# Optimization experiments

Measured on AMD Instinct MI355X. Metric: run time of the kernel, lower is better.

Reference implementation:

```python
import jax, jax.numpy as jnp
import numpy as np

# Config mirrors Model(d_model=512, output_dim=2); RetNet(num_layers=2, n_heads=1)
D_MODEL = 512
N_LAYERS = 2
OUT_DIM = 2
B, S = 16, 1024
GAMMA = 1.0 - 2.0 ** -5  # RetNet decay for head 0 (n_heads=1)
EPS = 1e-6


def setup_inputs() -> dict:
    key = jax.random.key(0)
    ks = jax.random.split(key, 10)
    d, L = D_MODEL, N_LAYERS

    def rn(k, shape, scale):
        return jax.random.normal(k, shape, dtype=jnp.float32) * scale

    return {
        "x": rn(ks[0], (B, S, d), 1.0),
        # per-layer retention projections, stacked on a leading layer axis
        "Wq": rn(ks[1], (L, d, d), d ** -0.5),
        "Wk": rn(ks[2], (L, d, d), d ** -0.5),
        "Wv": rn(ks[3], (L, d, d), d ** -0.5),
        "Wg": rn(ks[4], (L, d, d), d ** -0.5),
        "Wo": rn(ks[5], (L, d, d), d ** -0.5),
        # pre-norm LayerNorm affine params
        "ln1_g": jnp.ones((L, d), jnp.float32),
        "ln1_b": jnp.zeros((L, d), jnp.float32),
        "ln2_g": jnp.ones((L, d), jnp.float32),
        "ln2_b": jnp.zeros((L, d), jnp.float32),
        # FFN (hidden = 2*d_model, gelu) per RetNet paper
        "W1": rn(ks[6], (L, d, 2 * d), d ** -0.5),
        "b1": jnp.zeros((L, 2 * d), jnp.float32),
        "W2": rn(ks[7], (L, 2 * d, d), (2 * d) ** -0.5),
        "b2": jnp.zeros((L, d), jnp.float32),
        # readout Linear(d_model, output_dim)
        "Wro": rn(ks[8], (d, OUT_DIM), d ** -0.5),
        "bro": jnp.zeros((OUT_DIM,), jnp.float32),
    }


def _layer_norm(x, g, b):
    mu = jnp.mean(x, axis=-1, keepdims=True)
    var = jnp.var(x, axis=-1, keepdims=True)
    return (x - mu) * jax.lax.rsqrt(var + EPS) * g + b


def _retention(x, Wq, Wk, Wv, Wg, Wo):
    # single head: d_head = d_model
    d = x.shape[-1]
    q = x @ Wq                      # [B,S,d]
    k = (x @ Wk) * (d ** -0.5)      # scaled keys
    v = x @ Wv
    n = jnp.arange(x.shape[1])
    diff = n[:, None] - n[None, :]
    # D[n,m] = gamma^(n-m) for n >= m else 0 (causal decay mask)
    D = jnp.where(diff >= 0, jnp.exp(diff.astype(jnp.float32) * np.log(GAMMA)), 0.0)
    scores = jnp.einsum("bnd,bmd->bnm", q, k) * D       # [B,S,S]
    ret = jnp.einsum("bnm,bmd->bnd", scores, v)          # [B,S,d]
    # GroupNorm over the (single) head dim, no affine
    mu = jnp.mean(ret, axis=-1, keepdims=True)
    var = jnp.var(ret, axis=-1, keepdims=True)
    ret = (ret - mu) * jax.lax.rsqrt(var + EPS)
    # swish gate + output projection
    return (jax.nn.silu(x @ Wg) * ret) @ Wo


def reference(x, Wq, Wk, Wv, Wg, Wo, ln1_g, ln1_b, ln2_g, ln2_b, W1, b1, W2, b2, Wro, bro):
    h = x
    for l in range(N_LAYERS):  # small fixed layer count
        h = h + _retention(_layer_norm(h, ln1_g[l], ln1_b[l]), Wq[l], Wk[l], Wv[l], Wg[l], Wo[l])
        y = _layer_norm(h, ln2_g[l], ln2_b[l])
        h = h + jax.nn.gelu(y @ W1[l] + b1[l]) @ W2[l] + b2[l]
    pooled = h.sum(axis=1)          # [B,d] sum pooling over sequence
    return pooled @ Wro + bro       # [B,OUT_DIM]
```

## Files before the change

kernel.cpp:

```cpp
#include <hip/hip_runtime.h>
#include <hip/hip_bf16.h>


#define D_MODEL 512
#define SEQ 1024
#define BATCH 16
#define NROWS (BATCH * SEQ)
#define HID 1024
#define LOG2_GAMMA (-0.04580368961f)
#define KSCALE (0.044194173824f)

typedef __attribute__((ext_vector_type(8))) short bf16x8;
typedef __attribute__((ext_vector_type(4))) float f32x4;

__device__ inline unsigned short f2bf(float x) {
    union { float f; unsigned u; } uu; uu.f = x;
    unsigned r = uu.u + 0x7fff + ((uu.u >> 16) & 1);
    return (unsigned short)(r >> 16);
}
__device__ inline float bf2f(unsigned short x) {
    union { unsigned u; float f; } uu; uu.u = ((unsigned)x) << 16; return uu.f;
}

__device__ inline void gload_lds16(const void* g, void* l) {
    __builtin_amdgcn_global_load_lds(
        (const __attribute__((address_space(1))) void*)g,
        (__attribute__((address_space(3))) void*)l, 16, 0, 0);
}

__device__ inline float sigm(float z) {
    return 1.f / (1.f + exp2f(z * -1.442695040888963f));
}
__device__ inline float gelu_fast(float x) {
    float y = 1.5957691216057308f * (x + 0.044715f * x * x * x);
    return x * sigm(y);
}

template <int EPI>
__global__ __launch_bounds__(512, 2) void gemm256p(
    const short* __restrict__ A, const short* __restrict__ B,
    const float* __restrict__ bias, unsigned short* __restrict__ C,
    int K, int lda, int ldb, int ldc, int nbx) {
    __shared__ __align__(16) short smem[4 * 16384];
    const int tid = threadIdx.x;
    const int lane = tid & 63;
    const int wid = tid >> 6;
    const int wm = wid >> 2, wn = wid & 3;
    const int cpx = gridDim.x >> 3;
    const int wg = ((int)blockIdx.x & 7) * cpx + ((int)blockIdx.x >> 3);
    const int m0 = (wg / nbx) * 256;
    const int n0 = (wg % nbx) * 256;

    const int srow = tid >> 2;
    const int scol = (((tid & 3) ^ ((tid >> 3) & 3)) * 8);
    auto stage = [&](int slot, int t) {
        int k0 = t * 32;
#pragma unroll
        for (int r = 0; r < 2; ++r) {
            gload_lds16(A + (long long)(m0 + r * 128 + srow) * lda + k0 + scol,
                        &smem[slot * 16384 + r * 4096 + wid * 512]);
            gload_lds16(B + (long long)(n0 + r * 128 + srow) * ldb + k0 + scol,
                        &smem[slot * 16384 + 8192 + r * 4096 + wid * 512]);
        }
    };

    const int NT = K >> 5;
    f32x4 acc[8][4] = {};
    const int sw8 = (((lane >> 4) ^ ((lane >> 1) & 3)) * 8);
    const int aoff = (wm * 128 + (lane & 15)) * 32 + sw8;
    const int boff = 8192 + (wn * 64 + (lane & 15)) * 32 + sw8;

    bf16x8 aR0[8], bR0[4], aR1[8], bR1[4];
    stage(0, 0); stage(1, 1); stage(2, 2);
    asm volatile("s_waitcnt vmcnt(8)" ::: "memory");
    __builtin_amdgcn_s_barrier();
#pragma unroll
    for (int m = 0; m < 8; ++m) aR0[m] = *(const bf16x8*)&smem[aoff + m * 512];
#pragma unroll
    for (int n = 0; n < 4; ++n) bR0[n] = *(const bf16x8*)&smem[boff + n * 512];

#define STEP256(T, AC, BC, AN, BN2)                                                   \
    {                                                                                 \
        int t = (T);                                                                  \
        if (t + 3 < NT) stage((t + 3) & 3, t + 3);                                    \
        if (t + 3 < NT)      asm volatile("s_waitcnt vmcnt(8)" ::: "memory");         \
        else if (t + 2 < NT) asm volatile("s_waitcnt vmcnt(4)" ::: "memory");         \
        else if (t + 1 < NT) asm volatile("s_waitcnt vmcnt(0)" ::: "memory");         \
        __builtin_amdgcn_s_barrier();                                                 \
        const int sb = ((t + 1) & 3) * 16384;                                         \
        const bool pre = (t + 1 < NT);                                                \
        _Pragma("unroll")                                                             \
        for (int q = 0; q < 4; ++q) {                                                 \
            if (pre) {                                                                \
                AN[2 * q] = *(const bf16x8*)&smem[sb + aoff + (2 * q) * 512];          \
                AN[2 * q + 1] = *(const bf16x8*)&smem[sb + aoff + (2 * q + 1) * 512];  \
                BN2[q] = *(const bf16x8*)&smem[sb + boff + q * 512];                   \
            }                                                                         \
            __builtin_amdgcn_s_setprio(1);                                            \
            _Pragma("unroll")                                                         \
            for (int n = 0; n < 4; ++n) {                                             \
                acc[2 * q][n] = __builtin_amdgcn_mfma_f32_16x16x32_bf16(AC[2 * q], BC[n], acc[2 * q][n], 0, 0, 0); \
                acc[2 * q + 1][n] = __builtin_amdgcn_mfma_f32_16x16x32_bf16(AC[2 * q + 1], BC[n], acc[2 * q + 1][n], 0, 0, 0); \
            }                                                                         \
            __builtin_amdgcn_s_setprio(0);                                            \
            __builtin_amdgcn_sched_barrier(0);                                        \
        }                                                                             \
        asm volatile("s_waitcnt lgkmcnt(0)" ::: "memory");                            \
        __builtin_amdgcn_sched_barrier(0);                                            \
    }

    for (int tt = 0; tt < NT; tt += 2) {
        STEP256(tt, aR0, bR0, aR1, bR1)
        STEP256(tt + 1, aR1, bR1, aR0, bR0)
    }
#undef STEP256

    const int ocol = lane & 15;
    const int orow4 = (lane >> 4) * 4;
    float bv[4];
    if (EPI == 2) {
#pragma unroll
        for (int n = 0; n < 4; ++n) bv[n] = bias[n0 + wn * 64 + n * 16 + ocol];
    }
#pragma unroll 1
    for (int half = 0; half < 2; ++half) {
        __syncthreads();
        if (wm == half) {
#pragma unroll
            for (int m = 0; m < 8; ++m)
#pragma unroll
                for (int n = 0; n < 4; ++n)
#pragma unroll
                    for (int rj = 0; rj < 4; ++rj) {
                        int lr = m * 16 + orow4 + rj;
                        int lc = wn * 64 + n * 16 + ocol;
                        float v = acc[m][n][rj];
                        if (EPI == 2) v = gelu_fast(v + bv[n]);
                        smem[lr * 256 + lc] = (short)f2bf(v);
                    }
        }
        __syncthreads();
#pragma unroll
        for (int p = 0; p < 8; ++p) {
            int s = p * 512 + tid;
            int row = s >> 5;
            int cc = (s & 31) * 8;
            *(int4*)&C[(long long)(m0 + half * 128 + row) * ldc + n0 + cc] =
                *(const int4*)&smem[row * 256 + cc];
        }
    }
}

template <int EPI>
__global__ __launch_bounds__(256, 2) void pgemm128(
    const short* __restrict__ A, const short* __restrict__ B,
    const float* __restrict__ bias, unsigned short* __restrict__ C,
    int K, int lda, int ldb, int ldc,
    long long sA, long long sB, long long sC, int tri) {
    __shared__ __align__(16) short smem[4 * 8192];
    const int tid = threadIdx.x;
    const int lane = tid & 63;
    const int wid = tid >> 6;
    const int wr = wid >> 1, wc = wid & 1;
    const int m0 = blockIdx.y * 128, n0 = blockIdx.x * 128;
    A += (long long)blockIdx.z * sA;
    B += (long long)blockIdx.z * sB;

    int Keff = K;
    int kstart = 0;
    if (tri) { int km = m0 + 128; if (km < Keff) Keff = km; }
    if (tri == 2) { int ks = m0 - 256; if (ks > 0) kstart = ks; }
    const int NT = (Keff - kstart) >> 5;

    auto stage = [&](int slot, int t) {
        int k0 = kstart + t * 32;
#pragma unroll
        for (int it = 0; it < 2; ++it) {
            int c = it * 256 + tid;
            int rr = c >> 2;
            int cc = ((c & 3) ^ ((c >> 3) & 3)) * 8;
            gload_lds16(A + (long long)(m0 + rr) * lda + k0 + cc,
                        &smem[slot * 8192 + (it * 256 + wid * 64) * 8]);
            gload_lds16(B + (long long)(n0 + rr) * ldb + k0 + cc,
                        &smem[slot * 8192 + 4096 + (it * 256 + wid * 64) * 8]);
        }
    };

    f32x4 acc[4][4] = {};
    const int sw8 = (((lane >> 4) ^ ((lane >> 1) & 3)) * 8);
    const int aoff = (wr * 64 + (lane & 15)) * 32 + sw8;
    const int boff = 4096 + (wc * 64 + (lane & 15)) * 32 + sw8;

    bf16x8 aR0[4], bR0[4], aR1[4], bR1[4];
    stage(0, 0); stage(1, 1); stage(2, 2);
    asm volatile("s_waitcnt vmcnt(8)" ::: "memory");
    __builtin_amdgcn_s_barrier();
#pragma unroll
    for (int m = 0; m < 4; ++m) aR0[m] = *(const bf16x8*)&smem[aoff + m * 512];
#pragma unroll
    for (int n = 0; n < 4; ++n) bR0[n] = *(const bf16x8*)&smem[boff + n * 512];

#define STEPP(T, AC, BC, AN, BN2)                                                     \
    {                                                                                 \
        int t = (T);                                                                  \
        if (t + 3 < NT) stage((t + 3) & 3, t + 3);                                    \
        if (t + 3 < NT)      asm volatile("s_waitcnt vmcnt(8)" ::: "memory");         \
        else if (t + 2 < NT) asm volatile("s_waitcnt vmcnt(4)" ::: "memory");         \
        else if (t + 1 < NT) asm volatile("s_waitcnt vmcnt(0)" ::: "memory");         \
        __builtin_amdgcn_s_barrier();                                                 \
        const int sb = ((t + 1) & 3) * 8192;                                          \
        const bool pre = (t + 1 < NT);                                                \
        _Pragma("unroll")                                                             \
        for (int q = 0; q < 4; ++q) {                                                 \
            if (pre) {                                                                \
                AN[q] = *(const bf16x8*)&smem[sb + aoff + q * 512];                    \
                BN2[q] = *(const bf16x8*)&smem[sb + boff + q * 512];                   \
            }                                                                         \
            __builtin_amdgcn_s_setprio(1);                                            \
            _Pragma("unroll")                                                         \
            for (int n = 0; n < 4; ++n)                                               \
                acc[q][n] = __builtin_amdgcn_mfma_f32_16x16x32_bf16(AC[q], BC[n], acc[q][n], 0, 0, 0); \
            __builtin_amdgcn_s_setprio(0);                                            \
            __builtin_amdgcn_sched_barrier(0);                                        \
        }                                                                             \
        asm volatile("s_waitcnt lgkmcnt(0)" ::: "memory");                            \
        __builtin_amdgcn_sched_barrier(0);                                            \
    }

    for (int tt = 0; tt < NT; tt += 2) {
        STEPP(tt, aR0, bR0, aR1, bR1)
        STEPP(tt + 1, aR1, bR1, aR0, bR0)
    }
#undef STEPP

    __syncthreads();
    const int orow = (lane >> 4) * 4;
    const int ocol = lane & 15;
    float bv[4];
    if (EPI >= 1) {
#pragma unroll
        for (int j = 0; j < 4; ++j) bv[j] = bias[n0 + wc * 64 + j * 16 + ocol];
    }
#pragma unroll
    for (int i = 0; i < 4; ++i)
#pragma unroll
        for (int j = 0; j < 4; ++j)
#pragma unroll
            for (int rj = 0; rj < 4; ++rj) {
                int lrow = wr * 64 + i * 16 + orow + rj;
                int lcol = wc * 64 + j * 16 + ocol;
                float val = acc[i][j][rj];
                if (EPI == 1) val += bv[j];
                if (EPI == 2) val = gelu_fast(val + bv[j]);
                smem[lrow * 128 + lcol] = (short)f2bf(val);
            }
    __syncthreads();
    const long long zoff = (long long)blockIdx.z * sC;
#pragma unroll
    for (int p = 0; p < 8; ++p) {
        int s = p * 256 + tid;
        int row = s >> 4;
        int cc = (s & 15) * 8;
        *(int4*)&C[zoff + (long long)(m0 + row) * ldc + n0 + cc] = *(const int4*)&smem[row * 128 + cc];
    }
}

__global__ __launch_bounds__(256, 2) void pdecay(
    const short* __restrict__ Q, const short* __restrict__ Kp,
    unsigned short* __restrict__ S, int lda, long long sA) {
    if (blockIdx.x > blockIdx.y) return;
    if (blockIdx.y > blockIdx.x + 2) return;
    const int q0 = blockIdx.y * 128;
    const int c0 = blockIdx.x * 128;
    unsigned short* Sb = S + (long long)blockIdx.z * SEQ * SEQ;
    __shared__ __align__(16) short smem[4 * 8192];
    const int tid = threadIdx.x;
    const int lane = tid & 63;
    const int wid = tid >> 6;
    const int wr = wid >> 1, wc = wid & 1;
    const short* Ab = Q + (long long)blockIdx.z * sA;
    const short* Bb = Kp + (long long)blockIdx.z * sA;

    auto stage = [&](int slot, int t) {
        int k0 = t * 32;
#pragma unroll
        for (int it = 0; it < 2; ++it) {
            int c = it * 256 + tid;
            int rr = c >> 2;
            int cc = ((c & 3) ^ ((c >> 3) & 3)) * 8;
            gload_lds16(Ab + (long long)(q0 + rr) * lda + k0 + cc,
                        &smem[slot * 8192 + (it * 256 + wid * 64) * 8]);
            gload_lds16(Bb + (long long)(c0 + rr) * lda + k0 + cc,
                        &smem[slot * 8192 + 4096 + (it * 256 + wid * 64) * 8]);
        }
    };

    const int NT = D_MODEL / 32;
    f32x4 acc[4][4] = {};
    const int sw8 = (((lane >> 4) ^ ((lane >> 1) & 3)) * 8);
    const int aoff = (wr * 64 + (lane & 15)) * 32 + sw8;
    const int boff = 4096 + (wc * 64 + (lane & 15)) * 32 + sw8;

    bf16x8 aR0[4], bR0[4], aR1[4], bR1[4];
    stage(0, 0); stage(1, 1); stage(2, 2);
    asm volatile("s_waitcnt vmcnt(8)" ::: "memory");
    __builtin_amdgcn_s_barrier();
#pragma unroll
    for (int m = 0; m < 4; ++m) aR0[m] = *(const bf16x8*)&smem[aoff + m * 512];
#pragma unroll
    for (int n = 0; n < 4; ++n) bR0[n] = *(const bf16x8*)&smem[boff + n * 512];

#define STEPD(T, AC, BC, AN, BN2)                                                     \
    {                                                                                 \
        int t = (T);                                                                  \
        if (t + 3 < NT) stage((t + 3) & 3, t + 3);                                    \
        if (t + 3 < NT)      asm volatile("s_waitcnt vmcnt(8)" ::: "memory");         \
        else if (t + 2 < NT) asm volatile("s_waitcnt vmcnt(4)" ::: "memory");         \
        else if (t + 1 < NT) asm volatile("s_waitcnt vmcnt(0)" ::: "memory");         \
        __builtin_amdgcn_s_barrier();                                                 \
        const int sb = ((t + 1) & 3) * 8192;                                          \
        const bool pre = (t + 1 < NT);                                                \
        _Pragma("unroll")                                                             \
        for (int q = 0; q < 4; ++q) {                                                 \
            if (pre) {                                                                \
                AN[q] = *(const bf16x8*)&smem[sb + aoff + q * 512];                    \
                BN2[q] = *(const bf16x8*)&smem[sb + boff + q * 512];                   \
            }                                                                         \
            __builtin_amdgcn_s_setprio(1);                                            \
            _Pragma("unroll")                                                         \
            for (int n = 0; n < 4; ++n)                                               \
                acc[q][n] = __builtin_amdgcn_mfma_f32_16x16x32_bf16(AC[q], BC[n], acc[q][n], 0, 0, 0); \
            __builtin_amdgcn_s_setprio(0);                                            \
            __builtin_amdgcn_sched_barrier(0);                                        \
        }                                                                             \
        asm volatile("s_waitcnt lgkmcnt(0)" ::: "memory");                            \
        __builtin_amdgcn_sched_barrier(0);                                            \
    }

    for (int tt = 0; tt < NT; tt += 2) {
        STEPD(tt, aR0, bR0, aR1, bR1)
        STEPD(tt + 1, aR1, bR1, aR0, bR0)
    }
#undef STEPD

    __syncthreads();
    const int orow = (lane >> 4) * 4;
    const int ocol = lane & 15;
#pragma unroll
    for (int i = 0; i < 4; ++i)
#pragma unroll
        for (int j = 0; j < 4; ++j)
#pragma unroll
            for (int rj = 0; rj < 4; ++rj) {
                int lrow = wr * 64 + i * 16 + orow + rj;
                int lcol = wc * 64 + j * 16 + ocol;
                int n = q0 + lrow, m = c0 + lcol;
                float w = (n >= m) ? exp2f((float)(n - m) * LOG2_GAMMA) * KSCALE : 0.f;
                smem[lrow * 128 + lcol] = (short)f2bf(acc[i][j][rj] * w);
            }
    __syncthreads();
#pragma unroll
    for (int p = 0; p < 8; ++p) {
        int s = p * 256 + tid;
        int row = s >> 4;
        int cc = (s & 15) * 8;
        *(int4*)&Sb[(long long)(q0 + row) * SEQ + c0 + cc] = *(const int4*)&smem[row * 128 + cc];
    }
}

__global__ __launch_bounds__(256) void wconv_all(
    const float* __restrict__ Wq, const float* __restrict__ Wk,
    const float* __restrict__ Wv, const float* __restrict__ Wg,
    const float* __restrict__ Wo, const float* __restrict__ W1,
    const float* __restrict__ W2,
    unsigned short* __restrict__ WqkvgT, unsigned short* __restrict__ WoT,
    unsigned short* __restrict__ W1T, unsigned short* __restrict__ W2T) {
    const long long dd = 512LL * 512;
    int z = blockIdx.z;
    int l = z / 7, w = z % 7;
    const float* src; unsigned short* dst; int K, N;
    switch (w) {
        case 0: src = Wq + l * dd; dst = WqkvgT + (long long)l * 4 * dd; K = 512; N = 512; break;
        case 1: src = Wk + l * dd; dst = WqkvgT + (long long)l * 4 * dd + dd; K = 512; N = 512; break;
        case 2: src = Wv + l * dd; dst = WqkvgT + (long long)l * 4 * dd + 2 * dd; K = 512; N = 512; break;
        case 3: src = Wg + l * dd; dst = WqkvgT + (long long)l * 4 * dd + 3 * dd; K = 512; N = 512; break;
        case 4: src = Wo + l * dd; dst = WoT + l * dd; K = 512; N = 512; break;
        case 5: src = W1 + (long long)l * 512 * 1024; dst = W1T + (long long)l * 512 * 1024; K = 512; N = 1024; break;
        default: src = W2 + (long long)l * 1024 * 512; dst = W2T + (long long)l * 1024 * 512; K = 1024; N = 512; break;
    }
    if ((int)blockIdx.x >= N / 64 || (int)blockIdx.y >= K / 64) return;
    __shared__ unsigned short t[64][65];
    int n0 = blockIdx.x * 64, k0 = blockIdx.y * 64;
    int tx = threadIdx.x & 63, ty = threadIdx.x >> 6;
#pragma unroll
    for (int i = 0; i < 16; ++i)
        t[ty + i * 4][tx] = f2bf(src[(long long)(k0 + ty + i * 4) * N + n0 + tx]);
    __syncthreads();
#pragma unroll
    for (int i = 0; i < 16; ++i)
        dst[(long long)(n0 + ty + i * 4) * K + k0 + tx] = t[tx][ty + i * 4];
}

__global__ __launch_bounds__(256) void vtrans(const unsigned short* __restrict__ in,
                                              unsigned short* __restrict__ out, int istride) {
    __shared__ unsigned short t[64][65];
    const unsigned short* pin = in + (long long)blockIdx.z * SEQ * istride;
    unsigned short* pout = out + (long long)blockIdx.z * D_MODEL * SEQ;
    int c0 = blockIdx.x * 64, r0 = blockIdx.y * 64;
    int tx = threadIdx.x & 63, ty = threadIdx.x >> 6;
#pragma unroll
    for (int i = 0; i < 16; ++i)
        t[ty + i * 4][tx] = pin[(long long)(r0 + ty + i * 4) * istride + c0 + tx];
    __syncthreads();
#pragma unroll
    for (int i = 0; i < 16; ++i)
        pout[(long long)(c0 + ty + i * 4) * SEQ + r0 + tx] = t[tx][ty + i * 4];
}

template <int MODE>
__global__ __launch_bounds__(256) void ln_fuse(
    const void* __restrict__ hin_v,
    const unsigned short* __restrict__ delta,
    const float* __restrict__ g, const float* __restrict__ b,
    unsigned short* __restrict__ hout,
    unsigned short* __restrict__ y) {
    int row = blockIdx.x * 4 + (threadIdx.x >> 6);
    int t = threadIdx.x & 63;
    float f[8];
    if (MODE == 2) {
        const float4* r4 = (const float4*)((const float*)hin_v + (long long)row * D_MODEL);
        float4 v0 = r4[2 * t], v1 = r4[2 * t + 1];
        f[0] = v0.x; f[1] = v0.y; f[2] = v0.z; f[3] = v0.w;
        f[4] = v1.x; f[5] = v1.y; f[6] = v1.z; f[7] = v1.w;
    } else {
        const unsigned short* hin = (const unsigned short*)hin_v;
        int4 hv = ((const int4*)(hin + (long long)row * D_MODEL))[t];
        const unsigned short* hu = (const unsigned short*)&hv;
#pragma unroll
        for (int k = 0; k < 8; ++k) f[k] = bf2f(hu[k]);
    }
    if (MODE == 1) {
        int4 dv = ((const int4*)(delta + (long long)row * D_MODEL))[t];
        const unsigned short* du = (const unsigned short*)&dv;
#pragma unroll
        for (int k = 0; k < 8; ++k) f[k] += bf2f(du[k]);
    }
    float s = 0.f, s2 = 0.f;
#pragma unroll
    for (int k = 0; k < 8; ++k) { s += f[k]; s2 += f[k] * f[k]; }
#pragma unroll
    for (int off = 32; off > 0; off >>= 1) {
        s += __shfl_down(s, off);
        s2 += __shfl_down(s2, off);
    }
    s = __shfl(s, 0); s2 = __shfl(s2, 0);
    float mu = s * (1.f / D_MODEL);
    float var = s2 * (1.f / D_MODEL) - mu * mu;
    float rs = rsqrtf(var + 1e-6f);
    if (MODE >= 1) {
        ushort4 ho[2];
        unsigned short* hp = (unsigned short*)ho;
#pragma unroll
        for (int k = 0; k < 8; ++k) hp[k] = f2bf(f[k]);
        ((int4*)(hout + (long long)row * D_MODEL))[t] = *(int4*)ho;
    }
    const float4* g4 = (const float4*)g;
    const float4* b4 = (const float4*)b;
    float4 ga = g4[2 * t], gb2 = g4[2 * t + 1];
    float4 ba = b4[2 * t], bb2 = b4[2 * t + 1];
    float gg[8] = {ga.x, ga.y, ga.z, ga.w, gb2.x, gb2.y, gb2.z, gb2.w};
    float bb[8] = {ba.x, ba.y, ba.z, ba.w, bb2.x, bb2.y, bb2.z, bb2.w};
    ushort4 yo[2];
    unsigned short* yp = (unsigned short*)yo;
#pragma unroll
    for (int k = 0; k < 8; ++k) yp[k] = f2bf((f[k] - mu) * rs * gg[k] + bb[k]);
    ((int4*)(y + (long long)row * D_MODEL))[t] = *(int4*)yo;
}

__global__ __launch_bounds__(256) void gate_bf16(const unsigned short* __restrict__ ret,
                                                 const unsigned short* __restrict__ g,
                                                 int gstride,
                                                 unsigned short* __restrict__ out) {
    int row = blockIdx.x * 4 + (threadIdx.x >> 6);
    int t = threadIdx.x & 63;
    int4 rv4 = ((const int4*)(ret + (long long)row * D_MODEL))[t];
    const unsigned short* ru = (const unsigned short*)&rv4;
    float f[8];
#pragma unroll
    for (int k = 0; k < 8; ++k) f[k] = bf2f(ru[k]);
    float s = 0.f, s2 = 0.f;
#pragma unroll
    for (int k = 0; k < 8; ++k) { s += f[k]; s2 += f[k] * f[k]; }
#pragma unroll
    for (int off = 32; off > 0; off >>= 1) {
        s += __shfl_down(s, off);
        s2 += __shfl_down(s2, off);
    }
    s = __shfl(s, 0); s2 = __shfl(s2, 0);
    float mu = s * (1.f / D_MODEL);
    float var = s2 * (1.f / D_MODEL) - mu * mu;
    float rs = rsqrtf(var + 1e-6f);
    int4 gv4 = ((const int4*)(g + (long long)row * gstride))[t];
    const unsigned short* gu = (const unsigned short*)&gv4;
    ushort4 o[2];
    unsigned short* op = (unsigned short*)o;
#pragma unroll
    for (int k = 0; k < 8; ++k) {
        float x = bf2f(gu[k]);
        op[k] = f2bf(x * sigm(x) * (f[k] - mu) * rs);
    }
    ((int4*)(out + (long long)row * D_MODEL))[t] = *(int4*)o;
}

__global__ __launch_bounds__(256) void pool_s1(const unsigned short* __restrict__ h,
                                               const unsigned short* __restrict__ d,
                                               float* __restrict__ partial) {
    int b = blockIdx.x >> 4, g = blockIdx.x & 15;
    long long base = ((long long)b * SEQ + g * 64) * D_MODEL;
    int cw = (threadIdx.x & 63) * 8;
    int rg = threadIdx.x >> 6;
    float a[8] = {};
    for (int r = rg; r < 64; r += 4) {
        long long o = base + (long long)r * D_MODEL + cw;
        int4 hv = *(const int4*)&h[o];
        int4 dv = *(const int4*)&d[o];
        const unsigned short* hp = (const unsigned short*)&hv;
        const unsigned short* dp = (const unsigned short*)&dv;
#pragma unroll
        for (int j = 0; j < 8; ++j) a[j] += bf2f(hp[j]) + bf2f(dp[j]);
    }
    __shared__ float red[4][512];
#pragma unroll
    for (int j = 0; j < 8; ++j) red[rg][cw + j] = a[j];
    __syncthreads();
#pragma unroll
    for (int cc = 0; cc < 2; ++cc) {
        int c = threadIdx.x * 2 + cc;
        partial[(long long)blockIdx.x * D_MODEL + c] =
            red[0][c] + red[1][c] + red[2][c] + red[3][c];
    }
}

__global__ __launch_bounds__(256) void pool_s2(const float* __restrict__ partial,
                                               float* __restrict__ pooled) {
    int idx = blockIdx.x * 256 + threadIdx.x;
    int b = idx >> 9, c = idx & 511;
    float s = 0.f;
#pragma unroll
    for (int g = 0; g < 16; ++g) s += partial[(long long)(b * 16 + g) * D_MODEL + c];
    pooled[idx] = s;
}

__global__ __launch_bounds__(64) void readout_kernel(const float* __restrict__ pooled,
                                                     const float* __restrict__ Wro,
                                                     const float* __restrict__ bro,
                                                     float* __restrict__ out) {
    int bo = blockIdx.x;
    int b = bo >> 1, o = bo & 1;
    int t = threadIdx.x;
    float s = 0.f;
    for (int i = t; i < D_MODEL; i += 64) s += pooled[b * D_MODEL + i] * Wro[i * 2 + o];
#pragma unroll
    for (int off = 32; off > 0; off >>= 1) s += __shfl_down(s, off);
    if (t == 0) out[b * 2 + o] = s + bro[o];
}

extern "C" void kernel_launch(void* const* d_in, const int* in_sizes, int n_in,
                              void* d_out, int out_size, void* d_ws, size_t ws_size,
                              hipStream_t stream) {
    const float* x = (const float*)d_in[0];
    const float* Wq = (const float*)d_in[1];
    const float* Wk = (const float*)d_in[2];
    const float* Wv = (const float*)d_in[3];
    const float* Wg = (const float*)d_in[4];
    const float* Wo = (const float*)d_in[5];
    const float* ln1_g = (const float*)d_in[6];
    const float* ln1_b = (const float*)d_in[7];
    const float* ln2_g = (const float*)d_in[8];
    const float* ln2_b = (const float*)d_in[9];
    const float* W1 = (const float*)d_in[10];
    const float* b1 = (const float*)d_in[11];
    const float* W2 = (const float*)d_in[12];
    const float* b2 = (const float*)d_in[13];
    const float* Wro = (const float*)d_in[14];
    const float* bro = (const float*)d_in[15];
    float* out = (float*)d_out;

    const long long NE = (long long)NROWS * D_MODEL;
    const long long dd = (long long)D_MODEL * D_MODEL;

    unsigned short* h = (unsigned short*)d_ws;
    unsigned short* y = h + NE;
    unsigned short* qkvg = y + NE;
    unsigned short* vT = qkvg + 4 * NE;
    unsigned short* gated = vT;
    unsigned short* ret = vT + NE;
    unsigned short* sg = ret + NE;
    float* pooled = (float*)(sg + 2 * NE);
    float* partial = pooled + 8192;
    unsigned short* wts = (unsigned short*)(partial + 256 * 512);
    unsigned short* WqkvgT = wts;
    unsigned short* WoT = WqkvgT + 2 * 4 * dd;
    unsigned short* W1T = WoT + 2 * dd;
    unsigned short* W2T = W1T + 2 * (long long)D_MODEL * HID;

    dim3 blk(256);
    wconv_all<<<dim3(16, 16, 14), blk, 0, stream>>>(Wq, Wk, Wv, Wg, Wo, W1, W2,
                                                    WqkvgT, WoT, W1T, W2T);

    for (int l = 0; l < 2; l++) {
        if (l == 0)
            ln_fuse<2><<<NROWS / 4, blk, 0, stream>>>(x, nullptr, ln1_g, ln1_b, h, y);
        else
            ln_fuse<1><<<NROWS / 4, blk, 0, stream>>>(h, ret, ln1_g + l * D_MODEL,
                                                      ln1_b + l * D_MODEL, h, y);
        gemm256p<0><<<512, 512, 0, stream>>>(
            (const short*)y, (const short*)(WqkvgT + (long long)l * 4 * dd), nullptr, qkvg,
            512, 512, 512, 2048, 8);
        vtrans<<<dim3(8, 16, BATCH), blk, 0, stream>>>(qkvg + 1024, vT, 2048);
        pdecay<<<dim3(8, 8, BATCH), blk, 0, stream>>>(
            (const short*)qkvg, (const short*)(qkvg + 512), sg, 2048, (long long)SEQ * 2048);
        pgemm128<0><<<dim3(4, 8, BATCH), blk, 0, stream>>>(
            (const short*)sg, (const short*)vT, nullptr, ret,
            SEQ, SEQ, SEQ, 512,
            (long long)SEQ * SEQ, (long long)D_MODEL * SEQ, (long long)SEQ * D_MODEL, 2);
        gate_bf16<<<NROWS / 4, blk, 0, stream>>>(ret, qkvg + 1536, 2048, gated);
        pgemm128<0><<<dim3(4, 128), blk, 0, stream>>>(
            (const short*)gated, (const short*)(WoT + l * dd), nullptr, sg,
            512, 512, 512, 512, 0, 0, 0, 0);
        ln_fuse<1><<<NROWS / 4, blk, 0, stream>>>(h, sg, ln2_g + l * D_MODEL,
                                                  ln2_b + l * D_MODEL, h, y);
        gemm256p<2><<<256, 512, 0, stream>>>(
            (const short*)y, (const short*)(W1T + (long long)l * D_MODEL * HID),
            b1 + l * HID, sg, 512, 512, 512, HID, 4);
        pgemm128<1><<<dim3(4, 128), blk, 0, stream>>>(
            (const short*)sg, (const short*)(W2T + (long long)l * HID * D_MODEL),
            b2 + l * D_MODEL, ret, HID, HID, HID, 512, 0, 0, 0, 0);
    }

    pool_s1<<<256, blk, 0, stream>>>(h, ret, partial);
    pool_s2<<<32, blk, 0, stream>>>(partial, pooled);
    readout_kernel<<<32, 64, 0, stream>>>(pooled, Wro, bro, out);
}
```

Baseline: 435.9 us.

## Fold LayerNorm into following GEMMs via row stats and weight column sums

Replaces the LayerNorm kernels that wrote a normalized copy y with a residual-add kernel that writes only h plus per-row (rstd, -mu*rstd) stats. The LN gain is folded into the converted weights, and per-column sums of g*W and b*W (+bias) are precomputed, so the QKVG and FFN1 GEMMs consume h directly and apply the affine correction in the epilogue. This removes a full bf16 activation write and read per LayerNorm. In exchange the epilogue does extra per-element math, and a new, serially looped colsums kernel runs per call. Numerics shift because the GEMM now runs on unnormalized bf16 h rather than normalized y, and the mean is subtracted after accumulation, which risks cancellation error.

New measurement: 461.5 us. 5.9% more time.

```diff
diff --git a/kernel.cpp b/kernel.cpp
--- a/kernel.cpp
+++ b/kernel.cpp
@@ -39,9 +39,12 @@
 template <int EPI>
 __global__ __launch_bounds__(512, 2) void gemm256p(
     const short* __restrict__ A, const short* __restrict__ B,
-    const float* __restrict__ bias, unsigned short* __restrict__ C,
-    int K, int lda, int ldb, int ldc, int nbx) {
+    unsigned short* __restrict__ C,
+    int K, int lda, int ldb, int ldc, int nbx,
+    const float2* __restrict__ stats, const float* __restrict__ s1,
+    const float* __restrict__ s2) {
     __shared__ __align__(16) short smem[4 * 16384];
+    __shared__ float2 rowst[256];
     const int tid = threadIdx.x;
     const int lane = tid & 63;
     const int wid = tid >> 6;
@@ -117,10 +120,13 @@
 
     const int ocol = lane & 15;
     const int orow4 = (lane >> 4) * 4;
-    float bv[4];
-    if (EPI == 2) {
-#pragma unroll
-        for (int n = 0; n < 4; ++n) bv[n] = bias[n0 + wn * 64 + n * 16 + ocol];
+    if (tid < 256) rowst[tid] = stats[m0 + tid];
+    float s1v[4], s2v[4];
+#pragma unroll
+    for (int n = 0; n < 4; ++n) {
+        int col = n0 + wn * 64 + n * 16 + ocol;
+        s1v[n] = s1[col];
+        s2v[n] = s2[col];
     }
 #pragma unroll 1
     for (int half = 0; half < 2; ++half) {
@@ -134,8 +140,9 @@
                     for (int rj = 0; rj < 4; ++rj) {
                         int lr = m * 16 + orow4 + rj;
                         int lc = wn * 64 + n * 16 + ocol;
-                        float v = acc[m][n][rj];
-                        if (EPI == 2) v = gelu_fast(v + bv[n]);
+                        float2 ab = rowst[half * 128 + lr];
+                        float v = ab.x * acc[m][n][rj] + ab.y * s1v[n] + s2v[n];
+                        if (EPI == 4) v = gelu_fast(v);
                         smem[lr * 256 + lc] = (short)f2bf(v);
                     }
         }
@@ -251,7 +258,6 @@
                 int lcol = wc * 64 + j * 16 + ocol;
                 float val = acc[i][j][rj];
                 if (EPI == 1) val += bv[j];
-                if (EPI == 2) val = gelu_fast(val + bv[j]);
                 smem[lrow * 128 + lcol] = (short)f2bf(val);
             }
     __syncthreads();
@@ -373,19 +379,21 @@
     const float* __restrict__ Wv, const float* __restrict__ Wg,
     const float* __restrict__ Wo, const float* __restrict__ W1,
     const float* __restrict__ W2,
+    const float* __restrict__ ln1_g, const float* __restrict__ ln2_g,
     unsigned short* __restrict__ WqkvgT, unsigned short* __restrict__ WoT,
     unsigned short* __restrict__ W1T, unsigned short* __restrict__ W2T) {
     const long long dd = 512LL * 512;
     int z = blockIdx.z;
     int l = z / 7, w = z % 7;
     const float* src; unsigned short* dst; int K, N;
+    const float* gv = nullptr;
     switch (w) {
-        case 0: src = Wq + l * dd; dst = WqkvgT + (long long)l * 4 * dd; K = 512; N = 512; break;
-        case 1: src = Wk + l * dd; dst = WqkvgT + (long long)l * 4 * dd + dd; K = 512; N = 512; break;
-        case 2: src = Wv + l * dd; dst = WqkvgT + (long long)l * 4 * dd + 2 * dd; K = 512; N = 512; break;
-        case 3: src = Wg + l * dd; dst = WqkvgT + (long long)l * 4 * dd + 3 * dd; K = 512; N = 512; break;
+        case 0: src = Wq + l * dd; dst = WqkvgT + (long long)l * 4 * dd; K = 512; N = 512; gv = ln1_g + l * 512; break;
+        case 1: src = Wk + l * dd; dst = WqkvgT + (long long)l * 4 * dd + dd; K = 512; N = 512; gv = ln1_g + l * 512; break;
+        case 2: src = Wv + l * dd; dst = WqkvgT + (long long)l * 4 * dd + 2 * dd; K = 512; N = 512; gv = ln1_g + l * 512; break;
+        case 3: src = Wg + l * dd; dst = WqkvgT + (long long)l * 4 * dd + 3 * dd; K = 512; N = 512; gv = ln1_g + l * 512; break;
         case 4: src = Wo + l * dd; dst = WoT + l * dd; K = 512; N = 512; break;
-        case 5: src = W1 + (long long)l * 512 * 1024; dst = W1T + (long long)l * 512 * 1024; K = 512; N = 1024; break;
+        case 5: src = W1 + (long long)l * 512 * 1024; dst = W1T + (long long)l * 512 * 1024; K = 512; N = 1024; gv = ln2_g + l * 512; break;
         default: src = W2 + (long long)l * 1024 * 512; dst = W2T + (long long)l * 1024 * 512; K = 1024; N = 512; break;
     }
     if ((int)blockIdx.x >= N / 64 || (int)blockIdx.y >= K / 64) return;
@@ -393,12 +401,49 @@
     int n0 = blockIdx.x * 64, k0 = blockIdx.y * 64;
     int tx = threadIdx.x & 63, ty = threadIdx.x >> 6;
 #pragma unroll
-    for (int i = 0; i < 16; ++i)
-        t[ty + i * 4][tx] = f2bf(src[(long long)(k0 + ty + i * 4) * N + n0 + tx]);
+    for (int i = 0; i < 16; ++i) {
+        int k = k0 + ty + i * 4;
+        float v = src[(long long)k * N + n0 + tx];
+        if (gv) v *= gv[k];
+        t[ty + i * 4][tx] = f2bf(v);
+    }
     __syncthreads();
 #pragma unroll
     for (int i = 0; i < 16; ++i)
         dst[(long long)(n0 + ty + i * 4) * K + k0 + tx] = t[tx][ty + i * 4];
+}
+
+__global__ __launch_bounds__(256) void colsums(
+    const float* __restrict__ Wq, const float* __restrict__ Wk,
+    const float* __restrict__ Wv, const float* __restrict__ Wg,
+    const float* __restrict__ W1, const float* __restrict__ b1,
+    const float* __restrict__ ln1_g, const float* __restrict__ ln1_b,
+    const float* __restrict__ ln2_g, const float* __restrict__ ln2_b,
+    float* __restrict__ s1q, float* __restrict__ s2q,
+    float* __restrict__ s1f, float* __restrict__ s2f) {
+    const long long dd = 512LL * 512;
+    int z = blockIdx.z;
+    int l = z / 5, w = z % 5;
+    const float* src; const float* g; const float* b; const float* extra = nullptr;
+    float* d1; float* d2; int N;
+    switch (w) {
+        case 0: src = Wq + l * dd; g = ln1_g + l * 512; b = ln1_b + l * 512; d1 = s1q + l * 2048; d2 = s2q + l * 2048; N = 512; break;
+        case 1: src = Wk + l * dd; g = ln1_g + l * 512; b = ln1_b + l * 512; d1 = s1q + l * 2048 + 512; d2 = s2q + l * 2048 + 512; N = 512; break;
+        case 2: src = Wv + l * dd; g = ln1_g + l * 512; b = ln1_b + l * 512; d1 = s1q + l * 2048 + 1024; d2 = s2q + l * 2048 + 1024; N = 512; break;
+        case 3: src = Wg + l * dd; g = ln1_g + l * 512; b = ln1_b + l * 512; d1 = s1q + l * 2048 + 1536; d2 = s2q + l * 2048 + 1536; N = 512; break;
+        default: src = W1 + (long long)l * 512 * 1024; g = ln2_g + l * 512; b = ln2_b + l * 512; d1 = s1f + l * 1024; d2 = s2f + l * 1024; extra = b1 + l * 1024; N = 1024; break;
+    }
+    int col = blockIdx.x * 256 + threadIdx.x;
+    if (col >= N) return;
+    float a1 = 0.f, a2 = 0.f;
+    for (int k = 0; k < 512; ++k) {
+        float v = src[(long long)k * N + col];
+        a1 += g[k] * v;
+        a2 += b[k] * v;
+    }
+    if (extra) a2 += extra[col];
+    d1[col] = a1;
+    d2[col] = a2;
 }
 
 __global__ __launch_bounds__(256) void vtrans(const unsigned short* __restrict__ in,
@@ -418,12 +463,11 @@
 }
 
 template <int MODE>
-__global__ __launch_bounds__(256) void ln_fuse(
+__global__ __launch_bounds__(256) void resadd_stats(
     const void* __restrict__ hin_v,
     const unsigned short* __restrict__ delta,
-    const float* __restrict__ g, const float* __restrict__ b,
     unsigned short* __restrict__ hout,
-    unsigned short* __restrict__ y) {
+    float2* __restrict__ stats) {
     int row = blockIdx.x * 4 + (threadIdx.x >> 6);
     int t = threadIdx.x & 63;
     float f[8];
@@ -438,8 +482,6 @@
         const unsigned short* hu = (const unsigned short*)&hv;
 #pragma unroll
         for (int k = 0; k < 8; ++k) f[k] = bf2f(hu[k]);
-    }
-    if (MODE == 1) {
         int4 dv = ((const int4*)(delta + (long long)row * D_MODEL))[t];
         const unsigned short* du = (const unsigned short*)&dv;
 #pragma unroll
@@ -457,24 +499,15 @@
     float mu = s * (1.f / D_MODEL);
     float var = s2 * (1.f / D_MODEL) - mu * mu;
     float rs = rsqrtf(var + 1e-6f);
-    if (MODE >= 1) {
-        ushort4 ho[2];
-        unsigned short* hp = (unsigned short*)ho;
-#pragma unroll
-        for (int k = 0; k < 8; ++k) hp[k] = f2bf(f[k]);
-        ((int4*)(hout + (long long)row * D_MODEL))[t] = *(int4*)ho;
-    }
-    const float4* g4 = (const float4*)g;
-    const float4* b4 = (const float4*)b;
-    float4 ga = g4[2 * t], gb2 = g4[2 * t + 1];
-    float4 ba = b4[2 * t], bb2 = b4[2 * t + 1];
-    float gg[8] = {ga.x, ga.y, ga.z, ga.w, gb2.x, gb2.y, gb2.z, gb2.w};
-    float bb[8] = {ba.x, ba.y, ba.z, ba.w, bb2.x, bb2.y, bb2.z, bb2.w};
-    ushort4 yo[2];
-    unsigned short* yp = (unsigned short*)yo;
-#pragma unroll
-    for (int k = 0; k < 8; ++k) yp[k] = f2bf((f[k] - mu) * rs * gg[k] + bb[k]);
-    ((int4*)(y + (long long)row * D_MODEL))[t] = *(int4*)yo;
+    ushort4 ho[2];
+    unsigned short* hp = (unsigned short*)ho;
+#pragma unroll
+    for (int k = 0; k < 8; ++k) hp[k] = f2bf(f[k]);
+    ((int4*)(hout + (long long)row * D_MODEL))[t] = *(int4*)ho;
+    if (t == 0) {
+        float2 st; st.x = rs; st.y = -rs * mu;
+        stats[row] = st;
+    }
 }
 
 __global__ __launch_bounds__(256) void gate_bf16(const unsigned short* __restrict__ ret,
@@ -590,15 +623,19 @@
     const long long dd = (long long)D_MODEL * D_MODEL;
 
     unsigned short* h = (unsigned short*)d_ws;
-    unsigned short* y = h + NE;
-    unsigned short* qkvg = y + NE;
+    unsigned short* qkvg = h + NE;
     unsigned short* vT = qkvg + 4 * NE;
     unsigned short* gated = vT;
     unsigned short* ret = vT + NE;
     unsigned short* sg = ret + NE;
     float* pooled = (float*)(sg + 2 * NE);
     float* partial = pooled + 8192;
-    unsigned short* wts = (unsigned short*)(partial + 256 * 512);
+    float2* stats = (float2*)(partial + 256 * 512);
+    float* s1q = (float*)(stats + NROWS);
+    float* s2q = s1q + 2 * 2048;
+    float* s1f = s2q + 2 * 2048;
+    float* s2f = s1f + 2 * 1024;
+    unsigned short* wts = (unsigned short*)(s2f + 2 * 1024);
     unsigned short* WqkvgT = wts;
     unsigned short* WoT = WqkvgT + 2 * 4 * dd;
     unsigned short* W1T = WoT + 2 * dd;
@@ -606,17 +643,20 @@
 
     dim3 blk(256);
     wconv_all<<<dim3(16, 16, 14), blk, 0, stream>>>(Wq, Wk, Wv, Wg, Wo, W1, W2,
+                                                    ln1_g, ln2_g,
                                                     WqkvgT, WoT, W1T, W2T);
+    colsums<<<dim3(4, 1, 10), blk, 0, stream>>>(Wq, Wk, Wv, Wg, W1, b1,
+                                                ln1_g, ln1_b, ln2_g, ln2_b,
+                                                s1q, s2q, s1f, s2f);
 
     for (int l = 0; l < 2; l++) {
         if (l == 0)
-            ln_fuse<2><<<NROWS / 4, blk, 0, stream>>>(x, nullptr, ln1_g, ln1_b, h, y);
+            resadd_stats<2><<<NROWS / 4, blk, 0, stream>>>(x, nullptr, h, stats);
         else
-            ln_fuse<1><<<NROWS / 4, blk, 0, stream>>>(h, ret, ln1_g + l * D_MODEL,
-                                                      ln1_b + l * D_MODEL, h, y);
-        gemm256p<0><<<512, 512, 0, stream>>>(
-            (const short*)y, (const short*)(WqkvgT + (long long)l * 4 * dd), nullptr, qkvg,
-            512, 512, 512, 2048, 8);
+            resadd_stats<1><<<NROWS / 4, blk, 0, stream>>>(h, ret, h, stats);
+        gemm256p<3><<<512, 512, 0, stream>>>(
+            (const short*)h, (const short*)(WqkvgT + (long long)l * 4 * dd), qkvg,
+            512, 512, 512, 2048, 8, stats, s1q + l * 2048, s2q + l * 2048);
         vtrans<<<dim3(8, 16, BATCH), blk, 0, stream>>>(qkvg + 1024, vT, 2048);
         pdecay<<<dim3(8, 8, BATCH), blk, 0, stream>>>(
             (const short*)qkvg, (const short*)(qkvg + 512), sg, 2048, (long long)SEQ * 2048);
@@ -628,11 +668,10 @@
         pgemm128<0><<<dim3(4, 128), blk, 0, stream>>>(
             (const short*)gated, (const short*)(WoT + l * dd), nullptr, sg,
             512, 512, 512, 512, 0, 0, 0, 0);
-        ln_fuse<1><<<NROWS / 4, blk, 0, stream>>>(h, sg, ln2_g + l * D_MODEL,
-                                                  ln2_b + l * D_MODEL, h, y);
-        gemm256p<2><<<256, 512, 0, stream>>>(
-            (const short*)y, (const short*)(W1T + (long long)l * D_MODEL * HID),
-            b1 + l * HID, sg, 512, 512, 512, HID, 4);
+        resadd_stats<1><<<NROWS / 4, blk, 0, stream>>>(h, sg, h, stats);
+        gemm256p<4><<<256, 512, 0, stream>>>(
+            (const short*)h, (const short*)(W1T + (long long)l * D_MODEL * HID), sg,
+            512, 512, 512, HID, 4, stats, s1f + l * 1024, s2f + l * 1024);
         pgemm128<1><<<dim3(4, 128), blk, 0, stream>>>(
             (const short*)sg, (const short*)(W2T + (long long)l * HID * D_MODEL),
             b2 + l * D_MODEL, ret, HID, HID, HID, 512, 0, 0, 0, 0);
```
